# Kernel optimization log

Measured on AMD Instinct MI355X. Metric: run time of the kernel, lower is better.

Reference implementation:

```python
import jax, jax.numpy as jnp
import numpy as np

N_NODES = 100000
N_EDGES = 1600000
IN_F, H1, H2, H3, H4, H5, H6, NC = 512, 512, 256, 64, 64, 64, 64, 40


def _linear_params(key, fan_in, fan_out):
    k1, k2 = jax.random.split(key)
    bound = 1.0 / np.sqrt(fan_in)
    W = jax.random.uniform(k1, (fan_in, fan_out), minval=-bound, maxval=bound, dtype=jnp.float32)
    b = jax.random.uniform(k2, (fan_out,), minval=-bound, maxval=bound, dtype=jnp.float32)
    return W, b


def setup_inputs() -> dict:
    key = jax.random.key(0)
    ks = jax.random.split(key, 10)
    x = jax.random.normal(ks[0], (N_NODES, IN_F), dtype=jnp.float32)
    src = jax.random.randint(ks[1], (N_EDGES,), 0, N_NODES, dtype=jnp.int32)
    dst = jax.random.randint(ks[2], (N_EDGES,), 0, N_NODES, dtype=jnp.int32)
    W1, b1 = _linear_params(ks[3], IN_F, H1)
    W2, b2 = _linear_params(ks[4], H1, H2)
    W3, b3 = _linear_params(ks[5], H2, H3)
    Wg1, bg1 = _linear_params(ks[6], H3, H4)
    Wg2, bg2 = _linear_params(ks[7], H4, H5)
    Wg3, bg3 = _linear_params(ks[8], H5, H6)
    Wg4, bg4 = _linear_params(ks[9], H6, NC)
    return {"x": x, "src": src, "dst": dst,
            "W1": W1, "b1": b1, "W2": W2, "b2": b2, "W3": W3, "b3": b3,
            "Wg1": Wg1, "bg1": bg1, "Wg2": Wg2, "bg2": bg2,
            "Wg3": Wg3, "bg3": bg3, "Wg4": Wg4, "bg4": bg4}


def _graph_conv(h, src, dst, norm_src, norm_dst, W, b):
    # DGL GraphConv, norm='both': D_dst^{-1/2} A D_src^{-1/2} H W + b
    msg = (h * norm_src[:, None])[src]            # [E, d] gather from source nodes
    agg = jax.ops.segment_sum(msg, dst, num_segments=N_NODES)  # scatter-add to dst
    agg = agg * norm_dst[:, None]
    return agg @ W + b


def reference(x, src, dst, W1, b1, W2, b2, W3, b3,
              Wg1, bg1, Wg2, bg2, Wg3, bg3, Wg4, bg4):
    ones = jnp.ones((N_EDGES,), dtype=jnp.float32)
    deg_out = jax.ops.segment_sum(ones, src, num_segments=N_NODES)
    deg_in = jax.ops.segment_sum(ones, dst, num_segments=N_NODES)
    norm_src = jax.lax.rsqrt(jnp.clip(deg_out, 1.0))
    norm_dst = jax.lax.rsqrt(jnp.clip(deg_in, 1.0))

    h = jax.nn.relu(x @ W1 + b1)
    h = jax.nn.relu(h @ W2 + b2)
    h = jax.nn.relu(h @ W3 + b3)
    h = jax.nn.relu(_graph_conv(h, src, dst, norm_src, norm_dst, Wg1, bg1))
    h = jax.nn.relu(_graph_conv(h, src, dst, norm_src, norm_dst, Wg2, bg2))
    h = jax.nn.relu(_graph_conv(h, src, dst, norm_src, norm_dst, Wg3, bg3))
    h = jax.nn.relu(_graph_conv(h, src, dst, norm_src, norm_dst, Wg4, bg4))
    return h
```

## Files before the change

### kernel.cpp

```cpp
#include <hip/hip_runtime.h>

#define N_NODES 100000
#define N_EDGES 1600000
#define M_PAD   100096
#define BCAP    64

typedef __bf16 bf16x8 __attribute__((ext_vector_type(8)));
typedef float  f32x4  __attribute__((ext_vector_type(4)));

__device__ __forceinline__ unsigned short f2bf(float f) {
  union { float f; unsigned u; } x; x.f = f;
  unsigned r = (x.u + 0x7FFFu + ((x.u >> 16) & 1u)) >> 16;
  return (unsigned short)r;
}

__device__ __forceinline__ void async_copy16(const void* g, void* l) {
  __builtin_amdgcn_global_load_lds((__attribute__((address_space(1))) void*)g,
                                   (__attribute__((address_space(3))) void*)l,
                                   16, 0, 0);
}


__global__ void cvt_x_kernel(const float* __restrict__ x, unsigned short* __restrict__ xb,
                             long n_real, long n_pad) {
  long e = ((long)blockIdx.x * 256 + threadIdx.x) * 4;
  if (e >= n_pad) return;
  ushort4 o;
  if (e < n_real) {
    float4 f = *(const float4*)(x + e);
    o.x = f2bf(f.x); o.y = f2bf(f.y); o.z = f2bf(f.z); o.w = f2bf(f.w);
  } else {
    o.x = 0; o.y = 0; o.z = 0; o.w = 0;
  }
  *(ushort4*)(xb + e) = o;
}

__global__ void cvt_wt_kernel(const float* __restrict__ W, unsigned short* __restrict__ Wt,
                              int K, int N, int Npad) {
  int idx = blockIdx.x * 256 + threadIdx.x;
  if (idx >= Npad * K) return;
  int n = idx / K, k = idx % K;
  Wt[idx] = (n < N) ? f2bf(W[(long)k * N + n]) : (unsigned short)0;
}

__global__ void bucket_fill_kernel(const int* __restrict__ src, const int* __restrict__ dst,
                                   int* __restrict__ hist,
                                   int* __restrict__ bucket, int nE) {
  int e = blockIdx.x * 256 + threadIdx.x;
  if (e < nE) {
    int s = src[e], d = dst[e];
    atomicAdd(&hist[N_NODES + s], 1);
    int p = atomicAdd(&hist[d], 1);
    if (p < BCAP) bucket[(size_t)d * BCAP + p] = s;
  }
}

__global__ void norms_kernel(const int* __restrict__ hist,
                             float* __restrict__ nsrc, float* __restrict__ ndst) {
  int i = blockIdx.x * 256 + threadIdx.x;
  if (i >= M_PAD) return;
  if (i < N_NODES) {
    nsrc[i] = rsqrtf(fmaxf((float)hist[N_NODES + i], 1.f));
    ndst[i] = rsqrtf(fmaxf((float)hist[i], 1.f));
  } else {
    nsrc[i] = 1.f;
  }
}

template <int BM, int BN, int BK, int EPI>
__launch_bounds__(256)
__global__ void gemm_bt(const unsigned short* __restrict__ A,
                        const unsigned short* __restrict__ Bt,
                        const float* __restrict__ bias,
                        const float* __restrict__ rowscale,
                        void* __restrict__ C, int K, int Nfull) {
  constexpr int WM = BM / 2, WN = BN / 2;
  constexpr int MI = WM / 16, NI = WN / 16;
  __shared__ __align__(16) unsigned short As[BM * BK];
  __shared__ __align__(16) unsigned short Bs[BN * BK];
  const int tid = threadIdx.x;
  const int wave = tid >> 6, lane = tid & 63;
  const int wm0 = (wave >> 1) * WM, wn0 = (wave & 1) * WN;
  const long rowBase = (long)blockIdx.y * BM;
  const int colBase = blockIdx.x * BN;
  const unsigned short* Ab = A + rowBase * K;
  const unsigned short* Bb = Bt + (long)colBase * K;
  f32x4 acc[MI][NI] = {};
  constexpr int ACH = BM * BK / 8;
  constexpr int BCH = BN * BK / 8;
  for (int k0 = 0; k0 < K; k0 += BK) {
#pragma unroll
    for (int c = tid; c < ACH; c += 256) {
      int r = (c * 8) / BK, cc = (c * 8) % BK;
      async_copy16(Ab + (long)r * K + k0 + cc, &As[c * 8]);
    }
#pragma unroll
    for (int c = tid; c < BCH; c += 256) {
      int r = (c * 8) / BK, cc = (c * 8) % BK;
      async_copy16(Bb + (long)r * K + k0 + cc, &Bs[c * 8]);
    }
    __syncthreads();
#pragma unroll
    for (int kk = 0; kk < BK; kk += 32) {
      bf16x8 af[MI], bfr[NI];
#pragma unroll
      for (int mi = 0; mi < MI; ++mi)
        af[mi] = *(const bf16x8*)&As[(wm0 + mi * 16 + (lane & 15)) * BK + kk + (lane >> 4) * 8];
#pragma unroll
      for (int ni = 0; ni < NI; ++ni)
        bfr[ni] = *(const bf16x8*)&Bs[(wn0 + ni * 16 + (lane & 15)) * BK + kk + (lane >> 4) * 8];
#pragma unroll
      for (int mi = 0; mi < MI; ++mi)
#pragma unroll
        for (int ni = 0; ni < NI; ++ni)
          acc[mi][ni] = __builtin_amdgcn_mfma_f32_16x16x32_bf16(af[mi], bfr[ni], acc[mi][ni], 0, 0, 0);
    }
    __syncthreads();
  }
  const int q = lane >> 4, c15 = lane & 15;
#pragma unroll
  for (int mi = 0; mi < MI; ++mi) {
#pragma unroll
    for (int ni = 0; ni < NI; ++ni) {
#pragma unroll
      for (int r = 0; r < 4; ++r) {
        long row = rowBase + wm0 + mi * 16 + q * 4 + r;
        int col = colBase + wn0 + ni * 16 + c15;
        float v = acc[mi][ni][r];
        if (EPI == 0) {
          v = fmaxf(v + bias[col], 0.f);
          ((unsigned short*)C)[row * Nfull + col] = f2bf(v);
        } else if (EPI == 1) {
          v = fmaxf(v + bias[col], 0.f) * rowscale[row];
          ((unsigned short*)C)[row * Nfull + col] = f2bf(v);
        } else {
          ((float*)C)[row * Nfull + col] = v;
        }
      }
    }
  }
}

template <int FINAL>
__global__ void aggregate_kernel(const float* __restrict__ t,
                                 const int* __restrict__ bucket, const int* __restrict__ cnt,
                                 const float* __restrict__ ndst, const float* __restrict__ nsrc,
                                 const float* __restrict__ bias,
                                 unsigned short* __restrict__ gout, float* __restrict__ dout) {
  int node = blockIdx.x * 4 + (threadIdx.x >> 6);
  int lane = threadIdx.x & 63;
  int r = lane >> 4;
  int c = (lane & 15) * 4;
  int n = min(cnt[node], BCAP);
  const int* bk = bucket + (size_t)node * BCAP;
  float4 acc = make_float4(0.f, 0.f, 0.f, 0.f);
  for (int i = r; i < n; i += 4) {
    int s = bk[i];
    float4 v = *(const float4*)(t + (size_t)s * 64 + c);
    acc.x += v.x; acc.y += v.y; acc.z += v.z; acc.w += v.w;
  }
  acc.x += __shfl_xor(acc.x, 16); acc.y += __shfl_xor(acc.y, 16);
  acc.z += __shfl_xor(acc.z, 16); acc.w += __shfl_xor(acc.w, 16);
  acc.x += __shfl_xor(acc.x, 32); acc.y += __shfl_xor(acc.y, 32);
  acc.z += __shfl_xor(acc.z, 32); acc.w += __shfl_xor(acc.w, 32);
  if (r == 0) {
    float nd = ndst[node];
    float v0 = fmaxf(nd * acc.x + bias[c + 0], 0.f);
    float v1 = fmaxf(nd * acc.y + bias[c + 1], 0.f);
    float v2 = fmaxf(nd * acc.z + bias[c + 2], 0.f);
    float v3 = fmaxf(nd * acc.w + bias[c + 3], 0.f);
    if (FINAL) {
      if (c < 40) {
        float* o = dout + (size_t)node * 40;
        o[c + 0] = v0; o[c + 1] = v1; o[c + 2] = v2; o[c + 3] = v3;
      }
    } else {
      float ns = nsrc[node];
      ushort4 o;
      o.x = f2bf(v0 * ns); o.y = f2bf(v1 * ns);
      o.z = f2bf(v2 * ns); o.w = f2bf(v3 * ns);
      *(ushort4*)(gout + (size_t)node * 64 + c) = o;
    }
  }
}


extern "C" void kernel_launch(void* const* d_in, const int* in_sizes, int n_in,
                              void* d_out, int out_size, void* d_ws, size_t ws_size,
                              hipStream_t stream) {
  (void)in_sizes; (void)n_in; (void)out_size; (void)ws_size;
  const float* x   = (const float*)d_in[0];
  const int* esrc  = (const int*)d_in[1];
  const int* edst  = (const int*)d_in[2];
  const float* W1  = (const float*)d_in[3];  const float* b1  = (const float*)d_in[4];
  const float* W2  = (const float*)d_in[5];  const float* b2  = (const float*)d_in[6];
  const float* W3  = (const float*)d_in[7];  const float* b3  = (const float*)d_in[8];
  const float* Wg1 = (const float*)d_in[9];  const float* bg1 = (const float*)d_in[10];
  const float* Wg2 = (const float*)d_in[11]; const float* bg2 = (const float*)d_in[12];
  const float* Wg3 = (const float*)d_in[13]; const float* bg3 = (const float*)d_in[14];
  const float* Wg4 = (const float*)d_in[15]; const float* bg4 = (const float*)d_in[16];
  float* out = (float*)d_out;

  char* ws = (char*)d_ws;
  size_t off = 0;
  auto alloc = [&](size_t bytes) -> void* {
    void* p = ws + off;
    off += (bytes + 255) & ~(size_t)255;
    return p;
  };

  unsigned short* xb = (unsigned short*)alloc((size_t)M_PAD * 512 * 2);
  unsigned short* h1 = (unsigned short*)alloc((size_t)M_PAD * 512 * 2);
  int*   bucket  = (int*)alloc((size_t)N_NODES * BCAP * 4);
  int*   hist    = (int*)alloc((size_t)2 * N_NODES * 4);
  float* nsrc    = (float*)alloc((size_t)M_PAD * 4);
  float* ndst    = (float*)alloc((size_t)N_NODES * 4);
  unsigned short* W1t  = (unsigned short*)alloc(512 * 512 * 2);
  unsigned short* W2t  = (unsigned short*)alloc(256 * 512 * 2);
  unsigned short* W3t  = (unsigned short*)alloc(64 * 256 * 2);
  unsigned short* Wg1t = (unsigned short*)alloc(64 * 64 * 2);
  unsigned short* Wg2t = (unsigned short*)alloc(64 * 64 * 2);
  unsigned short* Wg3t = (unsigned short*)alloc(64 * 64 * 2);
  unsigned short* Wg4t = (unsigned short*)alloc(64 * 64 * 2);

  unsigned short* h2 = xb;
  unsigned short* ga = (unsigned short*)((char*)xb + (size_t)M_PAD * 256 * 2);
  unsigned short* ab = (unsigned short*)((char*)ga + (size_t)M_PAD * 64 * 2);
  float*          tb = (float*)((char*)ab + (size_t)M_PAD * 64 * 2);

  hipMemsetAsync(hist, 0, (size_t)2 * N_NODES * 4, stream);

  cvt_x_kernel<<<(int)(((size_t)M_PAD * 512 / 4 + 255) / 256), 256, 0, stream>>>(
      x, xb, (long)N_NODES * 512, (long)M_PAD * 512);

  bucket_fill_kernel<<<N_EDGES / 256, 256, 0, stream>>>(esrc, edst, hist, bucket, N_EDGES);

  norms_kernel<<<(M_PAD + 255) / 256, 256, 0, stream>>>(hist, nsrc, ndst);

  cvt_wt_kernel<<<(512 * 512 + 255) / 256, 256, 0, stream>>>(W1, W1t, 512, 512, 512);
  cvt_wt_kernel<<<(256 * 512 + 255) / 256, 256, 0, stream>>>(W2, W2t, 512, 256, 256);
  cvt_wt_kernel<<<(64 * 256 + 255) / 256, 256, 0, stream>>>(W3, W3t, 256, 64, 64);
  cvt_wt_kernel<<<(64 * 64 + 255) / 256, 256, 0, stream>>>(Wg1, Wg1t, 64, 64, 64);
  cvt_wt_kernel<<<(64 * 64 + 255) / 256, 256, 0, stream>>>(Wg2, Wg2t, 64, 64, 64);
  cvt_wt_kernel<<<(64 * 64 + 255) / 256, 256, 0, stream>>>(Wg3, Wg3t, 64, 64, 64);
  cvt_wt_kernel<<<(64 * 64 + 255) / 256, 256, 0, stream>>>(Wg4, Wg4t, 64, 40, 64);

  const int GY = M_PAD / 128;

  gemm_bt<128, 128, 64, 0><<<dim3(4, GY), 256, 0, stream>>>(xb, W1t, b1, nullptr, h1, 512, 512);
  gemm_bt<128, 128, 64, 0><<<dim3(2, GY), 256, 0, stream>>>(h1, W2t, b2, nullptr, h2, 512, 256);
  gemm_bt<128, 64, 64, 1><<<dim3(1, GY), 256, 0, stream>>>(h2, W3t, b3, nsrc, ga, 256, 64);

  gemm_bt<128, 64, 64, 2><<<dim3(1, GY), 256, 0, stream>>>(ga, Wg1t, nullptr, nullptr, tb, 64, 64);
  aggregate_kernel<0><<<N_NODES / 4, 256, 0, stream>>>(tb, bucket, hist, ndst, nsrc, bg1, ab, nullptr);

  gemm_bt<128, 64, 64, 2><<<dim3(1, GY), 256, 0, stream>>>(ab, Wg2t, nullptr, nullptr, tb, 64, 64);
  aggregate_kernel<0><<<N_NODES / 4, 256, 0, stream>>>(tb, bucket, hist, ndst, nsrc, bg2, ga, nullptr);

  gemm_bt<128, 64, 64, 2><<<dim3(1, GY), 256, 0, stream>>>(ga, Wg3t, nullptr, nullptr, tb, 64, 64);
  aggregate_kernel<0><<<N_NODES / 4, 256, 0, stream>>>(tb, bucket, hist, ndst, nsrc, bg3, ab, nullptr);

  gemm_bt<128, 64, 64, 2><<<dim3(1, GY), 256, 0, stream>>>(ab, Wg4t, nullptr, nullptr, tb, 64, 64);
  aggregate_kernel<1><<<N_NODES / 4, 256, 0, stream>>>(tb, bucket, hist, ndst, nsrc, bg4, nullptr, out);
}
```

Before: 937.6 us.

## Merge edge bucketing, input cast and weight transposes into one prep kernel

Replaces the x cast, edge bucket fill and seven weight-transpose launches with one kernel whose block ranges do different jobs. The atomic-heavy edge bucketing can then overlap with the bandwidth-bound x conversion, and eight launches go away. The x cast now handles 8 elements per thread through a grid-stride loop, and edges are read two at a time. Block-role branching adds code, and the block-id split into roles is fixed by hand.

```diff
diff --git a/kernel.cpp b/kernel.cpp
--- a/kernel.cpp
+++ b/kernel.cpp
@@ -5,8 +5,16 @@
 #define M_PAD   100096
 #define BCAP    64
 
+#define EB 3125
+#define XB 4096
+#define WB 416
+#define X_REAL 51200000L
+#define X_PAD  ((long)M_PAD*512)
+#define WTOT   425984
+
 typedef __bf16 bf16x8 __attribute__((ext_vector_type(8)));
 typedef float  f32x4  __attribute__((ext_vector_type(4)));
+typedef unsigned short u16x8 __attribute__((ext_vector_type(8)));
 
 __device__ __forceinline__ unsigned short f2bf(float f) {
   union { float f; unsigned u; } x; x.f = f;
@@ -20,38 +28,55 @@
                                    16, 0, 0);
 }
 
-
-__global__ void cvt_x_kernel(const float* __restrict__ x, unsigned short* __restrict__ xb,
-                             long n_real, long n_pad) {
-  long e = ((long)blockIdx.x * 256 + threadIdx.x) * 4;
-  if (e >= n_pad) return;
-  ushort4 o;
-  if (e < n_real) {
-    float4 f = *(const float4*)(x + e);
-    o.x = f2bf(f.x); o.y = f2bf(f.y); o.z = f2bf(f.z); o.w = f2bf(f.w);
+__global__ void mega_prep_kernel(const int* __restrict__ src, const int* __restrict__ dst,
+                                 int* __restrict__ hist, int* __restrict__ bucket,
+                                 const float* __restrict__ x, unsigned short* __restrict__ xb,
+                                 const float* __restrict__ W1, unsigned short* __restrict__ W1t,
+                                 const float* __restrict__ W2, unsigned short* __restrict__ W2t,
+                                 const float* __restrict__ W3, unsigned short* __restrict__ W3t,
+                                 const float* __restrict__ Wg1, unsigned short* __restrict__ Wg1t,
+                                 const float* __restrict__ Wg2, unsigned short* __restrict__ Wg2t,
+                                 const float* __restrict__ Wg3, unsigned short* __restrict__ Wg3t,
+                                 const float* __restrict__ Wg4, unsigned short* __restrict__ Wg4t) {
+  const int bid = blockIdx.x;
+  const int tid = threadIdx.x;
+  if (bid < EB) {
+    int e2 = bid * 256 + tid;
+    int2 s2 = ((const int2*)src)[e2];
+    int2 d2 = ((const int2*)dst)[e2];
+    atomicAdd(&hist[N_NODES + s2.x], 1);
+    int p0 = atomicAdd(&hist[d2.x], 1);
+    if (p0 < BCAP) bucket[(size_t)d2.x * BCAP + p0] = s2.x;
+    atomicAdd(&hist[N_NODES + s2.y], 1);
+    int p1 = atomicAdd(&hist[d2.y], 1);
+    if (p1 < BCAP) bucket[(size_t)d2.y * BCAP + p1] = s2.y;
+  } else if (bid < EB + XB) {
+    const long stride = (long)XB * 256 * 8;
+    for (long e = ((long)(bid - EB) * 256 + tid) * 8; e < X_PAD; e += stride) {
+      u16x8 o;
+      if (e < X_REAL) {
+        float4 f0 = *(const float4*)(x + e);
+        float4 f1 = *(const float4*)(x + e + 4);
+        o[0] = f2bf(f0.x); o[1] = f2bf(f0.y); o[2] = f2bf(f0.z); o[3] = f2bf(f0.w);
+        o[4] = f2bf(f1.x); o[5] = f2bf(f1.y); o[6] = f2bf(f1.z); o[7] = f2bf(f1.w);
+      } else {
+        o = (u16x8)0;
+      }
+      *(u16x8*)(xb + e) = o;
+    }
   } else {
-    o.x = 0; o.y = 0; o.z = 0; o.w = 0;
-  }
-  *(ushort4*)(xb + e) = o;
-}
-
-__global__ void cvt_wt_kernel(const float* __restrict__ W, unsigned short* __restrict__ Wt,
-                              int K, int N, int Npad) {
-  int idx = blockIdx.x * 256 + threadIdx.x;
-  if (idx >= Npad * K) return;
-  int n = idx / K, k = idx % K;
-  Wt[idx] = (n < N) ? f2bf(W[(long)k * N + n]) : (unsigned short)0;
-}
-
-__global__ void bucket_fill_kernel(const int* __restrict__ src, const int* __restrict__ dst,
-                                   int* __restrict__ hist,
-                                   int* __restrict__ bucket, int nE) {
-  int e = blockIdx.x * 256 + threadIdx.x;
-  if (e < nE) {
-    int s = src[e], d = dst[e];
-    atomicAdd(&hist[N_NODES + s], 1);
-    int p = atomicAdd(&hist[d], 1);
-    if (p < BCAP) bucket[(size_t)d * BCAP + p] = s;
+    for (int idx = (bid - EB - XB) * 256 + tid; idx < WTOT; idx += WB * 256) {
+      const float* W; unsigned short* Wt; int K, N, local;
+      if (idx < 262144)      { W = W1;  Wt = W1t;  K = 512; N = 512; local = idx; }
+      else if (idx < 393216) { W = W2;  Wt = W2t;  K = 512; N = 256; local = idx - 262144; }
+      else if (idx < 409600) { W = W3;  Wt = W3t;  K = 256; N = 64;  local = idx - 393216; }
+      else if (idx < 413696) { W = Wg1; Wt = Wg1t; K = 64;  N = 64;  local = idx - 409600; }
+      else if (idx < 417792) { W = Wg2; Wt = Wg2t; K = 64;  N = 64;  local = idx - 413696; }
+      else if (idx < 421888) { W = Wg3; Wt = Wg3t; K = 64;  N = 64;  local = idx - 417792; }
+      else                   { W = Wg4; Wt = Wg4t; K = 64;  N = 40;  local = idx - 421888; }
+      int n = local / K, k = local % K;
+      Wt[local] = (n < N) ? f2bf(W[(long)k * N + n]) : (unsigned short)0;
+    }
   }
 }
 
@@ -230,20 +255,11 @@
 
   hipMemsetAsync(hist, 0, (size_t)2 * N_NODES * 4, stream);
 
-  cvt_x_kernel<<<(int)(((size_t)M_PAD * 512 / 4 + 255) / 256), 256, 0, stream>>>(
-      x, xb, (long)N_NODES * 512, (long)M_PAD * 512);
-
-  bucket_fill_kernel<<<N_EDGES / 256, 256, 0, stream>>>(esrc, edst, hist, bucket, N_EDGES);
+  mega_prep_kernel<<<EB + XB + WB, 256, 0, stream>>>(
+      esrc, edst, hist, bucket, x, xb,
+      W1, W1t, W2, W2t, W3, W3t, Wg1, Wg1t, Wg2, Wg2t, Wg3, Wg3t, Wg4, Wg4t);
 
   norms_kernel<<<(M_PAD + 255) / 256, 256, 0, stream>>>(hist, nsrc, ndst);
-
-  cvt_wt_kernel<<<(512 * 512 + 255) / 256, 256, 0, stream>>>(W1, W1t, 512, 512, 512);
-  cvt_wt_kernel<<<(256 * 512 + 255) / 256, 256, 0, stream>>>(W2, W2t, 512, 256, 256);
-  cvt_wt_kernel<<<(64 * 256 + 255) / 256, 256, 0, stream>>>(W3, W3t, 256, 64, 64);
-  cvt_wt_kernel<<<(64 * 64 + 255) / 256, 256, 0, stream>>>(Wg1, Wg1t, 64, 64, 64);
-  cvt_wt_kernel<<<(64 * 64 + 255) / 256, 256, 0, stream>>>(Wg2, Wg2t, 64, 64, 64);
-  cvt_wt_kernel<<<(64 * 64 + 255) / 256, 256, 0, stream>>>(Wg3, Wg3t, 64, 64, 64);
-  cvt_wt_kernel<<<(64 * 64 + 255) / 256, 256, 0, stream>>>(Wg4, Wg4t, 64, 40, 64);
 
   const int GY = M_PAD / 128;
 
```

Measured after the change: 955.5 us. No clear change (+1.9%).

## Overlap edge bucketing with first GEMM and widen x conversion to 8 elements

Applied to the files above, without the earlier changes.

The standalone bucket_fill kernel is folded into the first MLP GEMM launch as an extra grid column, so edge histogram and bucket building run concurrently with the largest GEMM instead of as a separate serialized kernel. The norms kernel moves after that GEMM. The x fp32-to-bf16 conversion now handles 8 elements per thread with 16-byte stores. This removes launch gaps and lets the atomic-heavy pass hide behind compute, but the edge blocks may be scheduled late or contend with GEMM blocks for memory bandwidth.

```diff
diff --git a/kernel.cpp b/kernel.cpp
--- a/kernel.cpp
+++ b/kernel.cpp
@@ -4,9 +4,12 @@
 #define N_EDGES 1600000
 #define M_PAD   100096
 #define BCAP    64
+#define X_REAL 51200000L
+#define X_PAD  ((long)M_PAD*512)
 
 typedef __bf16 bf16x8 __attribute__((ext_vector_type(8)));
 typedef float  f32x4  __attribute__((ext_vector_type(4)));
+typedef unsigned short u16x8 __attribute__((ext_vector_type(8)));
 
 __device__ __forceinline__ unsigned short f2bf(float f) {
   union { float f; unsigned u; } x; x.f = f;
@@ -21,18 +24,18 @@
 }
 
 
-__global__ void cvt_x_kernel(const float* __restrict__ x, unsigned short* __restrict__ xb,
-                             long n_real, long n_pad) {
-  long e = ((long)blockIdx.x * 256 + threadIdx.x) * 4;
-  if (e >= n_pad) return;
-  ushort4 o;
-  if (e < n_real) {
-    float4 f = *(const float4*)(x + e);
-    o.x = f2bf(f.x); o.y = f2bf(f.y); o.z = f2bf(f.z); o.w = f2bf(f.w);
+__global__ void cvt_x_kernel(const float* __restrict__ x, unsigned short* __restrict__ xb) {
+  long e = ((long)blockIdx.x * 256 + threadIdx.x) * 8;
+  u16x8 o;
+  if (e < X_REAL) {
+    float4 f0 = *(const float4*)(x + e);
+    float4 f1 = *(const float4*)(x + e + 4);
+    o[0] = f2bf(f0.x); o[1] = f2bf(f0.y); o[2] = f2bf(f0.z); o[3] = f2bf(f0.w);
+    o[4] = f2bf(f1.x); o[5] = f2bf(f1.y); o[6] = f2bf(f1.z); o[7] = f2bf(f1.w);
   } else {
-    o.x = 0; o.y = 0; o.z = 0; o.w = 0;
-  }
-  *(ushort4*)(xb + e) = o;
+    o = (u16x8)0;
+  }
+  *(u16x8*)(xb + e) = o;
 }
 
 __global__ void cvt_wt_kernel(const float* __restrict__ W, unsigned short* __restrict__ Wt,
@@ -41,18 +44,6 @@
   if (idx >= Npad * K) return;
   int n = idx / K, k = idx % K;
   Wt[idx] = (n < N) ? f2bf(W[(long)k * N + n]) : (unsigned short)0;
-}
-
-__global__ void bucket_fill_kernel(const int* __restrict__ src, const int* __restrict__ dst,
-                                   int* __restrict__ hist,
-                                   int* __restrict__ bucket, int nE) {
-  int e = blockIdx.x * 256 + threadIdx.x;
-  if (e < nE) {
-    int s = src[e], d = dst[e];
-    atomicAdd(&hist[N_NODES + s], 1);
-    int p = atomicAdd(&hist[d], 1);
-    if (p < BCAP) bucket[(size_t)d * BCAP + p] = s;
-  }
 }
 
 __global__ void norms_kernel(const int* __restrict__ hist,
@@ -67,13 +58,27 @@
   }
 }
 
-template <int BM, int BN, int BK, int EPI>
+template <int BM, int BN, int BK, int EPI, bool EDGES>
 __launch_bounds__(256)
 __global__ void gemm_bt(const unsigned short* __restrict__ A,
                         const unsigned short* __restrict__ Bt,
                         const float* __restrict__ bias,
                         const float* __restrict__ rowscale,
-                        void* __restrict__ C, int K, int Nfull) {
+                        void* __restrict__ C, int K, int Nfull,
+                        const int* __restrict__ esrc, const int* __restrict__ edst,
+                        int* __restrict__ hist, int* __restrict__ bucket) {
+  if constexpr (EDGES) {
+    if (blockIdx.x == gridDim.x - 1) {
+      const int stride = gridDim.y * 256;
+      for (int e = blockIdx.y * 256 + threadIdx.x; e < N_EDGES; e += stride) {
+        int s = esrc[e], d = edst[e];
+        atomicAdd(&hist[N_NODES + s], 1);
+        int p = atomicAdd(&hist[d], 1);
+        if (p < BCAP) bucket[(size_t)d * BCAP + p] = s;
+      }
+      return;
+    }
+  }
   constexpr int WM = BM / 2, WN = BN / 2;
   constexpr int MI = WM / 16, NI = WN / 16;
   __shared__ __align__(16) unsigned short As[BM * BK];
@@ -230,12 +235,7 @@
 
   hipMemsetAsync(hist, 0, (size_t)2 * N_NODES * 4, stream);
 
-  cvt_x_kernel<<<(int)(((size_t)M_PAD * 512 / 4 + 255) / 256), 256, 0, stream>>>(
-      x, xb, (long)N_NODES * 512, (long)M_PAD * 512);
-
-  bucket_fill_kernel<<<N_EDGES / 256, 256, 0, stream>>>(esrc, edst, hist, bucket, N_EDGES);
-
-  norms_kernel<<<(M_PAD + 255) / 256, 256, 0, stream>>>(hist, nsrc, ndst);
+  cvt_x_kernel<<<(int)(X_PAD / 8 / 256), 256, 0, stream>>>(x, xb);
 
   cvt_wt_kernel<<<(512 * 512 + 255) / 256, 256, 0, stream>>>(W1, W1t, 512, 512, 512);
   cvt_wt_kernel<<<(256 * 512 + 255) / 256, 256, 0, stream>>>(W2, W2t, 512, 256, 256);
@@ -247,19 +247,29 @@
 
   const int GY = M_PAD / 128;
 
-  gemm_bt<128, 128, 64, 0><<<dim3(4, GY), 256, 0, stream>>>(xb, W1t, b1, nullptr, h1, 512, 512);
-  gemm_bt<128, 128, 64, 0><<<dim3(2, GY), 256, 0, stream>>>(h1, W2t, b2, nullptr, h2, 512, 256);
-  gemm_bt<128, 64, 64, 1><<<dim3(1, GY), 256, 0, stream>>>(h2, W3t, b3, nsrc, ga, 256, 64);
-
-  gemm_bt<128, 64, 64, 2><<<dim3(1, GY), 256, 0, stream>>>(ga, Wg1t, nullptr, nullptr, tb, 64, 64);
+  gemm_bt<128, 128, 64, 0, true><<<dim3(5, GY), 256, 0, stream>>>(
+      xb, W1t, b1, nullptr, h1, 512, 512, esrc, edst, hist, bucket);
+
+  norms_kernel<<<(M_PAD + 255) / 256, 256, 0, stream>>>(hist, nsrc, ndst);
+
+  gemm_bt<128, 128, 64, 0, false><<<dim3(2, GY), 256, 0, stream>>>(
+      h1, W2t, b2, nullptr, h2, 512, 256, nullptr, nullptr, nullptr, nullptr);
+  gemm_bt<128, 64, 64, 1, false><<<dim3(1, GY), 256, 0, stream>>>(
+      h2, W3t, b3, nsrc, ga, 256, 64, nullptr, nullptr, nullptr, nullptr);
+
+  gemm_bt<128, 64, 64, 2, false><<<dim3(1, GY), 256, 0, stream>>>(
+      ga, Wg1t, nullptr, nullptr, tb, 64, 64, nullptr, nullptr, nullptr, nullptr);
   aggregate_kernel<0><<<N_NODES / 4, 256, 0, stream>>>(tb, bucket, hist, ndst, nsrc, bg1, ab, nullptr);
 
-  gemm_bt<128, 64, 64, 2><<<dim3(1, GY), 256, 0, stream>>>(ab, Wg2t, nullptr, nullptr, tb, 64, 64);
+  gemm_bt<128, 64, 64, 2, false><<<dim3(1, GY), 256, 0, stream>>>(
+      ab, Wg2t, nullptr, nullptr, tb, 64, 64, nullptr, nullptr, nullptr, nullptr);
   aggregate_kernel<0><<<N_NODES / 4, 256, 0, stream>>>(tb, bucket, hist, ndst, nsrc, bg2, ga, nullptr);
 
-  gemm_bt<128, 64, 64, 2><<<dim3(1, GY), 256, 0, stream>>>(ga, Wg3t, nullptr, nullptr, tb, 64, 64);
+  gemm_bt<128, 64, 64, 2, false><<<dim3(1, GY), 256, 0, stream>>>(
+      ga, Wg3t, nullptr, nullptr, tb, 64, 64, nullptr, nullptr, nullptr, nullptr);
   aggregate_kernel<0><<<N_NODES / 4, 256, 0, stream>>>(tb, bucket, hist, ndst, nsrc, bg3, ab, nullptr);
 
-  gemm_bt<128, 64, 64, 2><<<dim3(1, GY), 256, 0, stream>>>(ab, Wg4t, nullptr, nullptr, tb, 64, 64);
+  gemm_bt<128, 64, 64, 2, false><<<dim3(1, GY), 256, 0, stream>>>(
+      ab, Wg4t, nullptr, nullptr, tb, 64, 64, nullptr, nullptr, nullptr, nullptr);
   aggregate_kernel<1><<<N_NODES / 4, 256, 0, stream>>>(tb, bucket, hist, ndst, nsrc, bg4, nullptr, out);
 }
```

Result: faster. 893.9 us (-4.7%).
